# Kernel tuning notes

Hardware: AMD Instinct MI355X
Metric: run time of the kernel (lower is better)

The kernel has to match this reference:

```python
import jax, jax.numpy as jnp
import numpy as np

ALPHA = 0.2  # LeakyReLU negative slope


def setup_inputs() -> dict:
    key = jax.random.key(0)
    k1, k2, k3, k4 = jax.random.split(key, 4)
    N, IN, H, D = 4096, 256, 8, 32
    h = jax.random.normal(k1, (N, IN), dtype=jnp.float32)
    adj = jax.random.randint(k2, (N, N), 0, 2, dtype=jnp.int32)
    W = jax.random.normal(k3, (H, IN, D), dtype=jnp.float32) * 0.074  # ~xavier gain 1.414
    a = jax.random.normal(k4, (H, 2 * D, 1), dtype=jnp.float32) * 0.23
    return {"h": h, "adj": adj, "W": W, "a": a}


def reference(h, adj, W, a):
    # h: [N, IN], adj: [N, N], W: [H, IN, D], a: [H, 2D, 1]
    H, IN, D = W.shape
    Wh = jnp.einsum('ni,hid->hnd', h, W)              # [H, N, D]
    a1 = a[:, :D, 0]                                   # [H, D]
    a2 = a[:, D:, 0]                                   # [H, D]
    Wh1 = jnp.einsum('hnd,hd->hn', Wh, a1)             # [H, N]
    Wh2 = jnp.einsum('hnd,hd->hn', Wh, a2)             # [H, N]
    e = Wh1[:, :, None] + Wh2[:, None, :]              # [H, N, N]
    e = jax.nn.leaky_relu(e, negative_slope=ALPHA)
    mask = (adj > 0)[None, :, :]                       # [1, N, N]
    e = jnp.where(mask, e, -jnp.inf)
    attention = jax.nn.softmax(e, axis=-1)             # [H, N, N]
    # dropout omitted (eval mode / deterministic)
    h_prime = jnp.einsum('hij,hjd->hid', attention, Wh)  # [H, N, D]
    # concat heads: [N, H*D]
    N = h.shape[0]
    return jnp.transpose(h_prime, (1, 0, 2)).reshape(N, H * D)
```

## Files before the change

kernel.cpp:

```cpp
#include <hip/hip_runtime.h>
#include <hip/hip_bf16.h>
#include <stdint.h>

#define GAT_ALPHA 0.2f
#define LOG2E 1.4426950408889634f

typedef __attribute__((ext_vector_type(8))) short bf16x8;
typedef __attribute__((ext_vector_type(8))) unsigned short ushort8;
typedef __attribute__((ext_vector_type(4))) float f32x4;
typedef __attribute__((ext_vector_type(4))) unsigned int u32x4;

#if __has_builtin(__builtin_amdgcn_exp2f)
#define EXP2F(x) __builtin_amdgcn_exp2f(x)
#else
#define EXP2F(x) exp2f(x)
#endif

static __device__ __forceinline__ unsigned int cvt_pk_bf16(float a, float b) {
    unsigned int r;
    asm("v_cvt_pk_bf16_f32 %0, %1, %2" : "=v"(r) : "v"(a), "v"(b));
    return r;
}

static __device__ __forceinline__ void gl16(const void* g, void* l) {
    __builtin_amdgcn_global_load_lds((const __attribute__((address_space(1))) void*)g,
                                     (__attribute__((address_space(3))) void*)l, 16, 0, 0);
}

__global__ __launch_bounds__(256) void k_pack_adj(const int* __restrict__ adj,
                                                  unsigned long long* __restrict__ packed,
                                                  int nwords,
                                                  const float* __restrict__ W,
                                                  unsigned short* __restrict__ wbfT) {
    int gid = blockIdx.x * 256 + threadIdx.x;
    int wid = gid >> 6;
    int lane = threadIdx.x & 63;
    if (wid < nwords) {
        int v = adj[(size_t)wid * 64 + lane];
        unsigned long long m = __ballot(v > 0);
        if (lane == 0) packed[wid] = m;
    }
    if (blockIdx.x < 32) {
        int idx = (blockIdx.x * 256 + threadIdx.x) * 8;
        int hd = idx >> 8;
        int i0 = idx & 255;
        int hh = hd >> 5, dd = hd & 31;
        float vv[8];
        #pragma unroll
        for (int k = 0; k < 8; ++k) vv[k] = W[((size_t)hh * 256 + i0 + k) * 32 + dd];
        u32x4 o = { cvt_pk_bf16(vv[0], vv[1]), cvt_pk_bf16(vv[2], vv[3]),
                    cvt_pk_bf16(vv[4], vv[5]), cvt_pk_bf16(vv[6], vv[7]) };
        *(u32x4*)&wbfT[idx] = o;
    }
}

__global__ __launch_bounds__(256) void k_wh2(const float* __restrict__ hmat,
                                             const unsigned short* __restrict__ wbfT,
                                             const float* __restrict__ avec,
                                             float* __restrict__ wh1s,
                                             float* __restrict__ wh2s,
                                             unsigned short* __restrict__ whT) {
    const int head = blockIdx.y;
    const int nbase = blockIdx.x * 64;
    const int t = threadIdx.x, w = t >> 6, lane = t & 63;
    const int r = lane & 15, q = lane >> 4;
    const int node0 = nbase + w * 16;

    f32x4 acc0 = {0.f, 0.f, 0.f, 0.f};
    f32x4 acc1 = {0.f, 0.f, 0.f, 0.f};
    const float* arow = &hmat[(size_t)(node0 + r) * 256];
    const unsigned short* b0p = &wbfT[((size_t)head * 32 + r) * 256];
    const unsigned short* b1p = b0p + 16 * 256;
    #pragma unroll
    for (int kt = 0; kt < 8; ++kt) {
        const int ko = kt * 32 + q * 8;
        float4 h0 = *(const float4*)&arow[ko];
        float4 h1 = *(const float4*)&arow[ko + 4];
        u32x4 ap = { cvt_pk_bf16(h0.x, h0.y), cvt_pk_bf16(h0.z, h0.w),
                     cvt_pk_bf16(h1.x, h1.y), cvt_pk_bf16(h1.z, h1.w) };
        bf16x8 af = __builtin_bit_cast(bf16x8, ap);
        bf16x8 b0 = *(const bf16x8*)&b0p[ko];
        bf16x8 b1 = *(const bf16x8*)&b1p[ko];
        acc0 = __builtin_amdgcn_mfma_f32_16x16x32_bf16(af, b0, acc0, 0, 0, 0);
        acc1 = __builtin_amdgcn_mfma_f32_16x16x32_bf16(af, b1, acc1, 0, 0, 0);
    }
    u32x4 pk = { cvt_pk_bf16(acc0[0], acc0[1]), cvt_pk_bf16(acc0[2], acc0[3]),
                 cvt_pk_bf16(acc1[0], acc1[1]), cvt_pk_bf16(acc1[2], acc1[3]) };
    unsigned long long lo = ((unsigned long long)pk[1] << 32) | pk[0];
    unsigned long long hi = ((unsigned long long)pk[3] << 32) | pk[2];
    *(unsigned long long*)&whT[((size_t)head * 32 + r) * 4096 + node0 + q * 4] = lo;
    *(unsigned long long*)&whT[((size_t)head * 32 + 16 + r) * 4096 + node0 + q * 4] = hi;

    float a1lo = avec[head * 64 + r],      a1hi = avec[head * 64 + 16 + r];
    float a2lo = avec[head * 64 + 32 + r], a2hi = avec[head * 64 + 48 + r];
    f32x4 d1, d2;
    #pragma unroll
    for (int i = 0; i < 4; ++i) {
        d1[i] = fmaf(acc0[i], a1lo, acc1[i] * a1hi);
        d2[i] = fmaf(acc0[i], a2lo, acc1[i] * a2hi);
    }
    #pragma unroll
    for (int s = 1; s < 16; s <<= 1) {
        #pragma unroll
        for (int i = 0; i < 4; ++i) {
            d1[i] += __shfl_xor(d1[i], s);
            d2[i] += __shfl_xor(d2[i], s);
        }
    }
    if (r == 0) {
        f32x4 o1 = d1 * LOG2E, o2 = d2 * LOG2E;
        *(f32x4*)&wh1s[(size_t)head * 4096 + node0 + q * 4] = o1;
        *(f32x4*)&wh2s[(size_t)head * 4096 + node0 + q * 4] = o2;
    }
}

__global__ __launch_bounds__(256, 4) void k_attn(const unsigned long long* __restrict__ adj64,
                                                 const float* __restrict__ wh1s,
                                                 const float* __restrict__ wh2s,
                                                 const unsigned short* __restrict__ whT,
                                                 float* __restrict__ out) {
    const int head = blockIdx.y;
    const int rowbase = blockIdx.x * 32;
    const int t = threadIdx.x;
    const int w = t >> 6;
    const int lane = t & 63;
    const int rt = w & 1;
    const int jh = w >> 1;
    const int r = lane & 15;
    const int q = lane >> 4;
    const int row = rowbase + rt * 16 + r;

    __shared__ unsigned short whTl[2][2][32][128];
    __shared__ float wh2t[2][2][128];
    __shared__ float wmxb[4];
    __shared__ unsigned int lut[256][4] __attribute__((aligned(16)));

    {
        unsigned int b = t;
        lut[t][0] = ((b & 1u)   ? 0xffffu : 0u) | ((b & 2u)   ? 0xffff0000u : 0u);
        lut[t][1] = ((b & 4u)   ? 0xffffu : 0u) | ((b & 8u)   ? 0xffff0000u : 0u);
        lut[t][2] = ((b & 16u)  ? 0xffffu : 0u) | ((b & 32u)  ? 0xffff0000u : 0u);
        lut[t][3] = ((b & 64u)  ? 0xffffu : 0u) | ((b & 128u) ? 0xffff0000u : 0u);
    }

    const int ghh = w >> 1;
    const int grg = (w & 1) * 4;
    const unsigned short* gsrc[4];
    #pragma unroll
    for (int c = 0; c < 4; ++c) {
        int d = (grg + c) * 4 + (lane >> 4);
        int p = lane & 15;
        int ls = (p & 8) | ((p ^ d) & 7);
        gsrc[c] = whT + ((size_t)(head * 32 + d)) * 4096 + ghh * 2048 + ls * 8;
    }
    const float* wh2p = &wh2s[(size_t)head * 4096];
    const float* wh2src = wh2p + (lane >> 5) * 2048 + (lane & 31) * 4;

    #pragma unroll
    for (int c = 0; c < 4; ++c)
        gl16(gsrc[c], &whTl[0][ghh][(grg + c) * 4][0]);
    if (w == 0) gl16(wh2src, &wh2t[0][0][0]);

    float lm = -INFINITY;
    #pragma unroll
    for (int kk = 0; kk < 4; ++kk) {
        float4 v = *(const float4*)&wh2p[kk * 1024 + t * 4];
        lm = fmaxf(fmaxf(lm, fmaxf(v.x, v.y)), fmaxf(v.z, v.w));
    }
    #pragma unroll
    for (int s = 1; s < 64; s <<= 1) lm = fmaxf(lm, __shfl_xor(lm, s));
    if (lane == 0) wmxb[w] = lm;
    __syncthreads();
    const float wm = fmaxf(fmaxf(wmxb[0], wmxb[1]), fmaxf(wmxb[2], wmxb[3]));

    const float wh1 = wh1s[(size_t)head * 4096 + row];
    const float sm0 = wh1 + wm;
    const float m = fmaxf(sm0, GAT_ALPHA * sm0);
    const float wh1m = wh1 - m;
    const float c2 = GAT_ALPHA * wh1 - m;

    f32x4 acc0 = {0.f, 0.f, 0.f, 0.f};
    f32x4 acc1 = {0.f, 0.f, 0.f, 0.f};
    f32x4 accd = {0.f, 0.f, 0.f, 0.f};

    const u32x4 onesu = {0x3F803F80u, 0x3F803F80u, 0x3F803F80u, 0x3F803F80u};
    const bf16x8 ones = __builtin_bit_cast(bf16x8, onesu);

    const unsigned long long* arow = adj64 + (size_t)row * 64 + jh * 32;
    unsigned long long au0 = arow[0], au1 = arow[1];
    int cur = 0;

    for (int step = 0; step < 16; ++step) {
        unsigned long long an0 = 0, an1 = 0;
        if (step < 15) {
            #pragma unroll
            for (int c = 0; c < 4; ++c)
                gl16(gsrc[c] + (step + 1) * 128, &whTl[cur ^ 1][ghh][(grg + c) * 4][0]);
            if (w == 0) gl16(wh2src + (step + 1) * 128, &wh2t[cur ^ 1][0][0]);
            an0 = arow[(step + 1) * 2];
            an1 = arow[(step + 1) * 2 + 1];
        }

        #pragma unroll
        for (int kk = 0; kk < 4; ++kk) {
            const int jl = kk * 32 + q * 8;
            const int slot = ((kk * 4 + q) ^ (r & 7)) * 8;
            bf16x8 b0 = *(const bf16x8*)&whTl[cur][jh][r][slot];
            bf16x8 b1 = *(const bf16x8*)&whTl[cur][jh][16 + r][slot];
            unsigned int bits =
                (unsigned int)(((kk < 2 ? au0 : au1) >> ((kk & 1) * 32 + q * 8)) & 0xffull);
            u32x4 mk = *(const u32x4*)lut[bits];
            float w2[8];
            *(float4*)&w2[0] = *(const float4*)&wh2t[cur][jh][jl];
            *(float4*)&w2[4] = *(const float4*)&wh2t[cur][jh][jl + 4];

            float p[8];
            #pragma unroll
            for (int b = 0; b < 8; ++b) {
                float u = wh1m + w2[b];
                float tv = fmaf(GAT_ALPHA, w2[b], c2);
                float s = fmaxf(u, tv);
                p[b] = EXP2F(s);
            }
            u32x4 pk = { cvt_pk_bf16(p[0], p[1]) & mk.x, cvt_pk_bf16(p[2], p[3]) & mk.y,
                         cvt_pk_bf16(p[4], p[5]) & mk.z, cvt_pk_bf16(p[6], p[7]) & mk.w };
            bf16x8 af = __builtin_bit_cast(bf16x8, pk);
            __builtin_amdgcn_s_setprio(1);
            acc0 = __builtin_amdgcn_mfma_f32_16x16x32_bf16(af, b0, acc0, 0, 0, 0);
            acc1 = __builtin_amdgcn_mfma_f32_16x16x32_bf16(af, b1, acc1, 0, 0, 0);
            accd = __builtin_amdgcn_mfma_f32_16x16x32_bf16(af, ones, accd, 0, 0, 0);
            __builtin_amdgcn_s_setprio(0);
        }

        __syncthreads();
        au0 = an0;
        au1 = an1;
        cur ^= 1;
    }

    f32x4* red = (f32x4*)whTl;
    if (jh == 1) {
        f32x4* rp = red + (rt * 64 + lane) * 3;
        rp[0] = acc0;
        rp[1] = acc1;
        rp[2] = accd;
    }
    __syncthreads();
    if (jh == 0) {
        const f32x4* rp = red + (rt * 64 + lane) * 3;
        acc0 += rp[0];
        acc1 += rp[1];
        accd += rp[2];
        #pragma unroll
        for (int i = 0; i < 4; ++i) {
            float inv = 1.0f / accd[i];
            int orow = rowbase + rt * 16 + 4 * q + i;
            out[(size_t)orow * 256 + head * 32 + r]      = acc0[i] * inv;
            out[(size_t)orow * 256 + head * 32 + 16 + r] = acc1[i] * inv;
        }
    }
}

extern "C" void kernel_launch(void* const* d_in, const int* in_sizes, int n_in,
                              void* d_out, int out_size, void* d_ws, size_t ws_size,
                              hipStream_t stream) {
    const float* h   = (const float*)d_in[0];
    const int*   adj = (const int*)d_in[1];
    const float* W   = (const float*)d_in[2];
    const float* a   = (const float*)d_in[3];
    float* out = (float*)d_out;

    char* ws = (char*)d_ws;
    unsigned long long* packed = (unsigned long long*)ws;
    float* wh1s = (float*)(ws + (2 << 20));
    float* wh2s = (float*)(ws + (2 << 20) + (128 << 10));
    unsigned short* whT  = (unsigned short*)(ws + (2 << 20) + (256 << 10));
    unsigned short* wbfT = (unsigned short*)(ws + (4 << 20) + (256 << 10));

    const int nwords = 4096 * 64;
    k_pack_adj<<<nwords * 64 / 256, 256, 0, stream>>>(adj, packed, nwords, W, wbfT);
    k_wh2<<<dim3(64, 8), 256, 0, stream>>>(h, wbfT, a, wh1s, wh2s, whT);
    k_attn<<<dim3(128, 8), 256, 0, stream>>>(packed, wh1s, wh2s, whT, out);
}
```

Baseline: 76.00 us.

## Factor exponentials into per-row and per-column fp16 terms, switch to f16 MFMA

Because exp2(max(a,b)) equals max(exp2(a), exp2(b)), the attention weight factors into a per-row scale times a per-column exponential. The per-column exponentials are computed once per block and stored in LDS as fp16, so the inner loop needs only packed fp16 multiplies and a max instead of 8 exp2 calls per lane. Wh and the probabilities move from bf16 to fp16 so that f16 MFMA can be used. The cost is reduced dynamic range: fp16 can overflow or underflow, and the column-only shift by wm may lose small probabilities.

```diff
diff --git a/kernel.cpp b/kernel.cpp
--- a/kernel.cpp
+++ b/kernel.cpp
@@ -6,6 +6,7 @@
 #define LOG2E 1.4426950408889634f
 
 typedef __attribute__((ext_vector_type(8))) short bf16x8;
+typedef __attribute__((ext_vector_type(8))) _Float16 f16x8;
 typedef __attribute__((ext_vector_type(8))) unsigned short ushort8;
 typedef __attribute__((ext_vector_type(4))) float f32x4;
 typedef __attribute__((ext_vector_type(4))) unsigned int u32x4;
@@ -84,10 +85,15 @@
         acc0 = __builtin_amdgcn_mfma_f32_16x16x32_bf16(af, b0, acc0, 0, 0, 0);
         acc1 = __builtin_amdgcn_mfma_f32_16x16x32_bf16(af, b1, acc1, 0, 0, 0);
     }
-    u32x4 pk = { cvt_pk_bf16(acc0[0], acc0[1]), cvt_pk_bf16(acc0[2], acc0[3]),
-                 cvt_pk_bf16(acc1[0], acc1[1]), cvt_pk_bf16(acc1[2], acc1[3]) };
-    unsigned long long lo = ((unsigned long long)pk[1] << 32) | pk[0];
-    unsigned long long hi = ((unsigned long long)pk[3] << 32) | pk[2];
+    auto ph = [](float x) {
+        return (unsigned int)__builtin_bit_cast(unsigned short, (_Float16)x);
+    };
+    unsigned int pk0 = ph(acc0[0]) | (ph(acc0[1]) << 16);
+    unsigned int pk1 = ph(acc0[2]) | (ph(acc0[3]) << 16);
+    unsigned int pk2 = ph(acc1[0]) | (ph(acc1[1]) << 16);
+    unsigned int pk3 = ph(acc1[2]) | (ph(acc1[3]) << 16);
+    unsigned long long lo = ((unsigned long long)pk1 << 32) | pk0;
+    unsigned long long hi = ((unsigned long long)pk3 << 32) | pk2;
     *(unsigned long long*)&whT[((size_t)head * 32 + r) * 4096 + node0 + q * 4] = lo;
     *(unsigned long long*)&whT[((size_t)head * 32 + 16 + r) * 4096 + node0 + q * 4] = hi;
 
@@ -131,7 +137,8 @@
     const int row = rowbase + rt * 16 + r;
 
     __shared__ unsigned short whTl[2][2][32][128];
-    __shared__ float wh2t[2][2][128];
+    __shared__ _Float16 e1t[2][2][128];
+    __shared__ _Float16 e2t[2][2][128];
     __shared__ float wmxb[4];
     __shared__ unsigned int lut[256][4] __attribute__((aligned(16)));
 
@@ -154,12 +161,9 @@
         gsrc[c] = whT + ((size_t)(head * 32 + d)) * 4096 + ghh * 2048 + ls * 8;
     }
     const float* wh2p = &wh2s[(size_t)head * 4096];
-    const float* wh2src = wh2p + (lane >> 5) * 2048 + (lane & 31) * 4;
-
-    #pragma unroll
-    for (int c = 0; c < 4; ++c)
-        gl16(gsrc[c], &whTl[0][ghh][(grg + c) * 4][0]);
-    if (w == 0) gl16(wh2src, &wh2t[0][0][0]);
+    const int ehh = t >> 7;
+    const int ejl = t & 127;
+    const float* esrc = wh2p + ehh * 2048 + ejl;
 
     float lm = -INFINITY;
     #pragma unroll
@@ -176,15 +180,28 @@
     const float wh1 = wh1s[(size_t)head * 4096 + row];
     const float sm0 = wh1 + wm;
     const float m = fmaxf(sm0, GAT_ALPHA * sm0);
-    const float wh1m = wh1 - m;
-    const float c2 = GAT_ALPHA * wh1 - m;
+    const _Float16 s1h = (_Float16)EXP2F(sm0 - m);
+    const _Float16 s2h = (_Float16)EXP2F(fmaf(GAT_ALPHA, sm0, -m));
+    f16x8 s1v, s2v;
+    #pragma unroll
+    for (int i = 0; i < 8; ++i) { s1v[i] = s1h; s2v[i] = s2h; }
+
+    #pragma unroll
+    for (int c = 0; c < 4; ++c)
+        gl16(gsrc[c], &whTl[0][ghh][(grg + c) * 4][0]);
+    {
+        float d0 = esrc[0] - wm;
+        e1t[0][ehh][ejl] = (_Float16)EXP2F(d0);
+        e2t[0][ehh][ejl] = (_Float16)EXP2F(GAT_ALPHA * d0);
+    }
+    __syncthreads();
 
     f32x4 acc0 = {0.f, 0.f, 0.f, 0.f};
     f32x4 acc1 = {0.f, 0.f, 0.f, 0.f};
     f32x4 accd = {0.f, 0.f, 0.f, 0.f};
 
-    const u32x4 onesu = {0x3F803F80u, 0x3F803F80u, 0x3F803F80u, 0x3F803F80u};
-    const bf16x8 ones = __builtin_bit_cast(bf16x8, onesu);
+    const u32x4 onesu = {0x3C003C00u, 0x3C003C00u, 0x3C003C00u, 0x3C003C00u};
+    const f16x8 ones = __builtin_bit_cast(f16x8, onesu);
 
     const unsigned long long* arow = adj64 + (size_t)row * 64 + jh * 32;
     unsigned long long au0 = arow[0], au1 = arow[1];
@@ -192,11 +209,12 @@
 
     for (int step = 0; step < 16; ++step) {
         unsigned long long an0 = 0, an1 = 0;
+        float vnext = 0.f;
         if (step < 15) {
             #pragma unroll
             for (int c = 0; c < 4; ++c)
                 gl16(gsrc[c] + (step + 1) * 128, &whTl[cur ^ 1][ghh][(grg + c) * 4][0]);
-            if (w == 0) gl16(wh2src + (step + 1) * 128, &wh2t[cur ^ 1][0][0]);
+            vnext = esrc[(step + 1) * 128];
             an0 = arow[(step + 1) * 2];
             an1 = arow[(step + 1) * 2 + 1];
         }
@@ -205,33 +223,29 @@
         for (int kk = 0; kk < 4; ++kk) {
             const int jl = kk * 32 + q * 8;
             const int slot = ((kk * 4 + q) ^ (r & 7)) * 8;
-            bf16x8 b0 = *(const bf16x8*)&whTl[cur][jh][r][slot];
-            bf16x8 b1 = *(const bf16x8*)&whTl[cur][jh][16 + r][slot];
+            f16x8 b0 = *(const f16x8*)&whTl[cur][jh][r][slot];
+            f16x8 b1 = *(const f16x8*)&whTl[cur][jh][16 + r][slot];
             unsigned int bits =
                 (unsigned int)(((kk < 2 ? au0 : au1) >> ((kk & 1) * 32 + q * 8)) & 0xffull);
             u32x4 mk = *(const u32x4*)lut[bits];
-            float w2[8];
-            *(float4*)&w2[0] = *(const float4*)&wh2t[cur][jh][jl];
-            *(float4*)&w2[4] = *(const float4*)&wh2t[cur][jh][jl + 4];
-
-            float p[8];
-            #pragma unroll
-            for (int b = 0; b < 8; ++b) {
-                float u = wh1m + w2[b];
-                float tv = fmaf(GAT_ALPHA, w2[b], c2);
-                float s = fmaxf(u, tv);
-                p[b] = EXP2F(s);
-            }
-            u32x4 pk = { cvt_pk_bf16(p[0], p[1]) & mk.x, cvt_pk_bf16(p[2], p[3]) & mk.y,
-                         cvt_pk_bf16(p[4], p[5]) & mk.z, cvt_pk_bf16(p[6], p[7]) & mk.w };
-            bf16x8 af = __builtin_bit_cast(bf16x8, pk);
+            f16x8 e1 = *(const f16x8*)&e1t[cur][jh][jl];
+            f16x8 e2 = *(const f16x8*)&e2t[cur][jh][jl];
+
+            f16x8 pp = __builtin_elementwise_max(s1v * e1, s2v * e2);
+            u32x4 pk = __builtin_bit_cast(u32x4, pp) & mk;
+            f16x8 af = __builtin_bit_cast(f16x8, pk);
             __builtin_amdgcn_s_setprio(1);
-            acc0 = __builtin_amdgcn_mfma_f32_16x16x32_bf16(af, b0, acc0, 0, 0, 0);
-            acc1 = __builtin_amdgcn_mfma_f32_16x16x32_bf16(af, b1, acc1, 0, 0, 0);
-            accd = __builtin_amdgcn_mfma_f32_16x16x32_bf16(af, ones, accd, 0, 0, 0);
+            acc0 = __builtin_amdgcn_mfma_f32_16x16x32_f16(af, b0, acc0, 0, 0, 0);
+            acc1 = __builtin_amdgcn_mfma_f32_16x16x32_f16(af, b1, acc1, 0, 0, 0);
+            accd = __builtin_amdgcn_mfma_f32_16x16x32_f16(af, ones, accd, 0, 0, 0);
             __builtin_amdgcn_s_setprio(0);
         }
 
+        if (step < 15) {
+            float d1v = vnext - wm;
+            e1t[cur ^ 1][ehh][ejl] = (_Float16)EXP2F(d1v);
+            e2t[cur ^ 1][ehh][ejl] = (_Float16)EXP2F(GAT_ALPHA * d1v);
+        }
         __syncthreads();
         au0 = an0;
         au1 = an1;
```

Result: faster. 69.28 us, median of 2 (-8.8%).
